# Performance work log

Hardware: AMD Instinct MI355X
Metric: run time of the kernel (lower is better)

The kernel has to match this reference:

```python
import jax, jax.numpy as jnp
import numpy as np
import math

HEAD_DIM = 128
N_HEADS = 32
N_KV_HEADS = 8
ROPE_THETA = 10000.0


def _rotate_half(x):
    x1, x2 = jnp.split(x, 2, axis=-1)
    return jnp.concatenate([-x2, x1], axis=-1)


def _rope_cos_sin(position_ids, head_dim, theta):
    # position_ids: [B, S] int
    inv_freq = 1.0 / (theta ** (jnp.arange(0, head_dim, 2, dtype=jnp.float32) / head_dim))
    freqs = position_ids.astype(jnp.float32)[..., None] * inv_freq[None, None, :]  # [B,S,D/2]
    emb = jnp.concatenate([freqs, freqs], axis=-1)  # [B,S,D]
    return jnp.cos(emb), jnp.sin(emb)


def setup_inputs() -> dict:
    key = jax.random.key(0)
    k1, k2, k3, k4, k5 = jax.random.split(key, 5)
    B, S, H = 1, 2048, 4096
    hidden_states = jax.random.normal(k1, (B, S, H), dtype=jnp.float32)
    Wq = jax.random.normal(k2, (N_HEADS * HEAD_DIM, H), dtype=jnp.float32) * (1.0 / math.sqrt(H))
    Wk = jax.random.normal(k3, (N_KV_HEADS * HEAD_DIM, H), dtype=jnp.float32) * (1.0 / math.sqrt(H))
    Wv = jax.random.normal(k4, (N_KV_HEADS * HEAD_DIM, H), dtype=jnp.float32) * (1.0 / math.sqrt(H))
    Wo = jax.random.normal(k5, (H, N_HEADS * HEAD_DIM), dtype=jnp.float32) * (1.0 / math.sqrt(H))
    position_ids = jnp.arange(S, dtype=jnp.int32)[None, :]
    return {"hidden_states": hidden_states, "Wq": Wq, "Wk": Wk, "Wv": Wv, "Wo": Wo,
            "position_ids": position_ids}


def reference(hidden_states, Wq, Wk, Wv, Wo, position_ids):
    B, S, H = hidden_states.shape
    d = HEAD_DIM
    groups = N_HEADS // N_KV_HEADS

    # projections (torch Linear: x @ W^T)
    q = (hidden_states @ Wq.T).reshape(B, S, N_HEADS, d).transpose(0, 2, 1, 3)      # [B,Hq,S,d]
    k = (hidden_states @ Wk.T).reshape(B, S, N_KV_HEADS, d).transpose(0, 2, 1, 3)   # [B,Hk,S,d]
    v = (hidden_states @ Wv.T).reshape(B, S, N_KV_HEADS, d).transpose(0, 2, 1, 3)

    cos, sin = _rope_cos_sin(position_ids, d, ROPE_THETA)  # [B,S,d]
    cos = cos[:, None, :, :]
    sin = sin[:, None, :, :]
    q = q * cos + _rotate_half(q) * sin
    k = k * cos + _rotate_half(k) * sin

    # GQA: repeat kv heads
    k = jnp.repeat(k, groups, axis=1)  # [B,Hq,S,d]
    v = jnp.repeat(v, groups, axis=1)

    scores = jnp.einsum('bhqd,bhkd->bhqk', q, k) / math.sqrt(d)
    causal = jnp.tril(jnp.ones((S, S), dtype=bool))
    scores = jnp.where(causal[None, None], scores, jnp.finfo(jnp.float32).min)
    attn = jax.nn.softmax(scores.astype(jnp.float32), axis=-1).astype(q.dtype)

    out = jnp.einsum('bhqk,bhkd->bhqd', attn, v)        # [B,Hq,S,d]
    out = out.transpose(0, 2, 1, 3).reshape(B, S, N_HEADS * d)
    return out @ Wo.T
```

## Files before the change

kernel.cpp:

```cpp
#include <hip/hip_runtime.h>
#include <hip/hip_bf16.h>
#include <cstdint>
#include <cstddef>

#define S_LEN 2048
#define HID   4096
#define HD    128
#define NH    32
#define NKV   8
#define KVW   (NKV * HD)
#define QKVN  (HID + 2 * KVW)

typedef __bf16 bf16x8_t __attribute__((ext_vector_type(8)));
typedef float  f32x4_t  __attribute__((ext_vector_type(4)));
typedef unsigned short u16x8_t __attribute__((ext_vector_type(8)));

__device__ __forceinline__ unsigned short f2b(float f) {
  unsigned u = __float_as_uint(f);
  u += 0x7FFFu + ((u >> 16) & 1u);
  return (unsigned short)(u >> 16);
}
__device__ __forceinline__ float b2f(unsigned short v) {
  return __uint_as_float(((unsigned)v) << 16);
}
__device__ __forceinline__ float fexp2(float x) {
  float r;
  asm("v_exp_f32 %0, %1" : "=v"(r) : "v"(x));
  return r;
}
__device__ __forceinline__ void gld_lds16(const void* g, void* l) {
  __builtin_amdgcn_global_load_lds(
      (const __attribute__((address_space(1))) void*)g,
      (__attribute__((address_space(3))) void*)l, 16, 0, 0);
}

__global__ void cvt4_kernel(const float* __restrict__ s0, const float* __restrict__ s1,
                            const float* __restrict__ s2, const float* __restrict__ s3,
                            unsigned short* __restrict__ dst) {
  const int B0 = 2097152;
  const int B1 = B0 + 4194304;
  const int B2 = B1 + 1048576;
  const int B3 = B2 + 1048576;
  int i = blockIdx.x * blockDim.x + threadIdx.x;
  int stride = gridDim.x * blockDim.x;
  for (; i < B3; i += stride) {
    const float* s; int off;
    if (i < B0)      { s = s0; off = i; }
    else if (i < B1) { s = s1; off = i - B0; }
    else if (i < B2) { s = s2; off = i - B1; }
    else             { s = s3; off = i - B2; }
    float4 v = reinterpret_cast<const float4*>(s)[off];
    ushort4 o;
    o.x = f2b(v.x); o.y = f2b(v.y); o.z = f2b(v.z); o.w = f2b(v.w);
    reinterpret_cast<ushort4*>(dst)[i] = o;
  }
}

#define QSCALE 0.12751744846f
__global__ void rope_kernel(unsigned short* __restrict__ Q,
                            unsigned short* __restrict__ Kb,
                            const int* __restrict__ pos_ids) {
  const int total = S_LEN * (NH + NKV) * 64;
  int idx = blockIdx.x * blockDim.x + threadIdx.x;
  int stride = gridDim.x * blockDim.x;
  for (; idx < total; idx += stride) {
    int s   = idx / ((NH + NKV) * 64);
    int rem = idx % ((NH + NKV) * 64);
    int hp  = rem >> 6;
    int i   = rem & 63;
    unsigned short* ptr; int W, h;
    if (hp < NH) { ptr = Q;  W = HID; h = hp; }
    else         { ptr = Kb; W = KVW; h = hp - NH; }
    float pos = (float)pos_ids[s];
    float ang = pos * __expf(-(float)i * 0.14391156516f);
    float sn, cs;
    sincosf(ang, &sn, &cs);
    size_t base = (size_t)s * W + (size_t)h * HD + i;
    float lo = b2f(ptr[base]);
    float hi = b2f(ptr[base + 64]);
    float o0 = lo * cs - hi * sn;
    float o1 = hi * cs + lo * sn;
    if (hp < NH) { o0 *= QSCALE; o1 *= QSCALE; }
    ptr[base]      = f2b(o0);
    ptr[base + 64] = f2b(o1);
  }
}

template <int BN, int MODE>
__global__ __launch_bounds__(512, 4) void gemm4p_kernel(
    const unsigned short* __restrict__ A, const unsigned short* __restrict__ B,
    void* __restrict__ C0, void* __restrict__ C1, void* __restrict__ C2,
    int N, int K) {
  constexpr int NFR = BN / 64;
  constexpr int ABYTES = 128 * 128;
  constexpr int TILE_LDS = ABYTES + BN * 128;
  __shared__ char ldsB[2 * TILE_LDS];

  const int tid  = threadIdx.x;
  const int lane = tid & 63;
  const int wid  = tid >> 6;
  const int wm = wid >> 2, wn = wid & 3;
  const int lr = lane & 15, g = lane >> 4;
  const int bm = blockIdx.y * 128;
  const int bn = blockIdx.x * BN;
  const int nk = K >> 6;
  const int ni = nk >> 1;
  const int xr = (lr & 7) << 4;

  auto stage_u = [&](int t, int u) {
    if (t >= nk) return;
    const int riu = tid >> 3;
    const int cbs = ((tid & 7) << 4) ^ ((riu & 7) << 4);
    const char* src;
    if (u < 2)
      src = (const char*)A + ((size_t)(bm + u * 64 + riu) * K + t * 64) * 2 + cbs;
    else
      src = (const char*)B + ((size_t)(bn + (u - 2) * 64 + riu) * K + t * 64) * 2 + cbs;
    gld_lds16(src, ldsB + (t & 1) * TILE_LDS + u * 8192 + tid * 16);
  };

  auto rdA = [&](const char* bb, int m, int k) {
    const int row = wm * 64 + m * 16 + lr;
    return *(const bf16x8_t*)(bb + row * 128 + ((k * 64 + g * 16) ^ xr));
  };
  auto rdB = [&](const char* bb, int n, int k) {
    const int row = wn * (BN / 4) + n * 16 + lr;
    return *(const bf16x8_t*)(bb + ABYTES + row * 128 + ((k * 64 + g * 16) ^ xr));
  };

  for (int t = 0; t < 2; ++t)
    for (int u = 0; u < 2 + NFR; ++u) stage_u(t, u);
  asm volatile("s_waitcnt vmcnt(0)" ::: "memory");
  __builtin_amdgcn_sched_barrier(0);
  __builtin_amdgcn_s_barrier();

  f32x4_t acc[4][NFR];
#pragma unroll
  for (int m = 0; m < 4; ++m)
#pragma unroll
    for (int n = 0; n < NFR; ++n) acc[m][n] = f32x4_t{0.f, 0.f, 0.f, 0.f};

  bf16x8_t bfr[NFR][2], af[2][2];

#define MFMA_BLOCK(MB)                                                        \
  __builtin_amdgcn_s_setprio(1);                                              \
  _Pragma("unroll") for (int m = 0; m < 2; ++m)                               \
    _Pragma("unroll") for (int n = 0; n < NFR; ++n)                           \
      _Pragma("unroll") for (int k = 0; k < 2; ++k)                           \
        acc[(MB) + m][n] = __builtin_amdgcn_mfma_f32_16x16x32_bf16(           \
            af[m][k], bfr[n][k], acc[(MB) + m][n], 0, 0, 0);                  \
  __builtin_amdgcn_s_setprio(0);

#define GATE()                                                                \
  __builtin_amdgcn_s_barrier();                                               \
  asm volatile("s_waitcnt lgkmcnt(0)" ::: "memory");                          \
  __builtin_amdgcn_sched_barrier(0);

#define RD_A2(bb, m0)                                                         \
  _Pragma("unroll") for (int m = 0; m < 2; ++m)                               \
    _Pragma("unroll") for (int k = 0; k < 2; ++k)                             \
      af[m][k] = rdA(bb, (m0) + m, k);

#define RD_B(bb)                                                              \
  _Pragma("unroll") for (int n = 0; n < NFR; ++n)                             \
    _Pragma("unroll") for (int k = 0; k < 2; ++k)                             \
      bfr[n][k] = rdB(bb, n, k);

  for (int i = 0; i < ni; ++i) {
    const char* bE = ldsB;
    const char* bO = ldsB + TILE_LDS;
    const int tO = 2 * i + 1, tE2 = 2 * i + 2, tO2 = 2 * i + 3;
    const bool last = (i == ni - 1);

    RD_B(bE);
    RD_A2(bE, 0);
    if (i > 0) { stage_u(tO, 0); stage_u(tO, 1); }
    GATE(); MFMA_BLOCK(0);
    __builtin_amdgcn_s_barrier();

    RD_A2(bE, 2);
#pragma unroll
    for (int u = 0; u < NFR; ++u) stage_u(tE2, 2 + u);
    GATE(); MFMA_BLOCK(2);
    if (last) { asm volatile("s_waitcnt vmcnt(0)" ::: "memory"); }
    else      { asm volatile("s_waitcnt vmcnt(%0)" :: "n"(NFR) : "memory"); }
    __builtin_amdgcn_sched_barrier(0);
    __builtin_amdgcn_s_barrier();

    RD_B(bO);
    RD_A2(bO, 0);
    stage_u(tE2, 0); stage_u(tE2, 1);
    GATE(); MFMA_BLOCK(0);
    __builtin_amdgcn_s_barrier();

    RD_A2(bO, 2);
#pragma unroll
    for (int u = 0; u < NFR; ++u) stage_u(tO2, 2 + u);
    GATE(); MFMA_BLOCK(2);
    if (!last) { asm volatile("s_waitcnt vmcnt(%0)" :: "n"(NFR) : "memory"); }
    __builtin_amdgcn_sched_barrier(0);
    __builtin_amdgcn_s_barrier();
  }
#undef MFMA_BLOCK
#undef GATE
#undef RD_A2
#undef RD_B

#pragma unroll
  for (int mf = 0; mf < 4; ++mf) {
    const int row0 = bm + wm * 64 + mf * 16 + g * 4;
#pragma unroll
    for (int nf = 0; nf < NFR; ++nf) {
      const int col = bn + wn * (BN / 4) + nf * 16 + lr;
      if constexpr (MODE == 1) {
#pragma unroll
        for (int r = 0; r < 4; ++r)
          ((float*)C0)[(size_t)(row0 + r) * N + col] = acc[mf][nf][r];
      } else {
        if (col < HID) {
#pragma unroll
          for (int r = 0; r < 4; ++r)
            ((unsigned short*)C0)[(size_t)(row0 + r) * HID + col] = f2b(acc[mf][nf][r]);
        } else if (col < HID + KVW) {
#pragma unroll
          for (int r = 0; r < 4; ++r)
            ((unsigned short*)C1)[(size_t)(row0 + r) * KVW + (col - HID)] = f2b(acc[mf][nf][r]);
        } else {
          const int c2 = col - HID - KVW;
          ushort4 w;
          w.x = f2b(acc[mf][nf][0]); w.y = f2b(acc[mf][nf][1]);
          w.z = f2b(acc[mf][nf][2]); w.w = f2b(acc[mf][nf][3]);
          *(ushort4*)(void*)&((unsigned short*)C2)[(size_t)c2 * S_LEN + row0] = w;
        }
      }
    }
  }
}

template <int BN, int MODE>
__global__ __launch_bounds__(256, 2) void gemm4w_kernel(
    const unsigned short* __restrict__ A, const unsigned short* __restrict__ B,
    void* __restrict__ C0, void* __restrict__ C1, void* __restrict__ C2,
    int N, int K) {
  constexpr int NFRW = BN / 32;
  constexpr int ABYTES = 128 * 128;
  constexpr int TILE_LDS = ABYTES + BN * 128;
  __shared__ char ldsB[2 * TILE_LDS];

  const int tid  = threadIdx.x;
  const int lane = tid & 63;
  const int wid  = tid >> 6;
  const int wm = wid >> 1, wn = wid & 1;
  const int lr = lane & 15, g = lane >> 4;
  const int bm = blockIdx.y * 128;
  const int bn = blockIdx.x * BN;
  const int nk = K >> 6;
  const int ni = nk >> 1;
  const int xr = (lr & 7) << 4;

  auto stage_u = [&](int t, int u) {
    if (t >= nk) return;
    const int riu = tid >> 3;
    const int cbs = ((tid & 7) << 4) ^ ((riu & 7) << 4);
    const char* src;
    if (u < 4)
      src = (const char*)A + ((size_t)(bm + u * 32 + riu) * K + t * 64) * 2 + cbs;
    else
      src = (const char*)B + ((size_t)(bn + (u - 4) * 32 + riu) * K + t * 64) * 2 + cbs;
    gld_lds16(src, ldsB + (t & 1) * TILE_LDS + u * 4096 + tid * 16);
  };

  auto rdA = [&](const char* bb, int m, int k) {
    const int row = wm * 64 + m * 16 + lr;
    return *(const bf16x8_t*)(bb + row * 128 + ((k * 64 + g * 16) ^ xr));
  };
  auto rdB = [&](const char* bb, int n, int k) {
    const int row = wn * (BN / 2) + n * 16 + lr;
    return *(const bf16x8_t*)(bb + ABYTES + row * 128 + ((k * 64 + g * 16) ^ xr));
  };

  for (int t = 0; t < 2; ++t)
    for (int u = 0; u < 4 + NFRW; ++u) stage_u(t, u);
  asm volatile("s_waitcnt vmcnt(0)" ::: "memory");
  __builtin_amdgcn_sched_barrier(0);
  __builtin_amdgcn_s_barrier();

  f32x4_t acc[4][NFRW];
#pragma unroll
  for (int m = 0; m < 4; ++m)
#pragma unroll
    for (int n = 0; n < NFRW; ++n) acc[m][n] = f32x4_t{0.f, 0.f, 0.f, 0.f};

  bf16x8_t bfr[NFRW][2], af[2][2];

#define MFMA_BLOCK(MB)                                                        \
  __builtin_amdgcn_s_setprio(1);                                              \
  _Pragma("unroll") for (int m = 0; m < 2; ++m)                               \
    _Pragma("unroll") for (int n = 0; n < NFRW; ++n)                          \
      _Pragma("unroll") for (int k = 0; k < 2; ++k)                           \
        acc[(MB) + m][n] = __builtin_amdgcn_mfma_f32_16x16x32_bf16(           \
            af[m][k], bfr[n][k], acc[(MB) + m][n], 0, 0, 0);                  \
  __builtin_amdgcn_s_setprio(0);

#define GATE()                                                                \
  __builtin_amdgcn_s_barrier();                                               \
  asm volatile("s_waitcnt lgkmcnt(0)" ::: "memory");                          \
  __builtin_amdgcn_sched_barrier(0);

#define RD_A2(bb, m0)                                                         \
  _Pragma("unroll") for (int m = 0; m < 2; ++m)                               \
    _Pragma("unroll") for (int k = 0; k < 2; ++k)                             \
      af[m][k] = rdA(bb, (m0) + m, k);

#define RD_B(bb)                                                              \
  _Pragma("unroll") for (int n = 0; n < NFRW; ++n)                            \
    _Pragma("unroll") for (int k = 0; k < 2; ++k)                             \
      bfr[n][k] = rdB(bb, n, k);

  for (int i = 0; i < ni; ++i) {
    const char* bE = ldsB;
    const char* bO = ldsB + TILE_LDS;
    const int tO = 2 * i + 1, tE2 = 2 * i + 2, tO2 = 2 * i + 3;
    const bool last = (i == ni - 1);

    RD_B(bE);
    RD_A2(bE, 0);
    if (i > 0) {
#pragma unroll
      for (int u = 0; u < 4; ++u) stage_u(tO, u);
    }
    GATE(); MFMA_BLOCK(0);
    __builtin_amdgcn_s_barrier();

    RD_A2(bE, 2);
#pragma unroll
    for (int u = 0; u < NFRW; ++u) stage_u(tE2, 4 + u);
    GATE(); MFMA_BLOCK(2);
    if (last) { asm volatile("s_waitcnt vmcnt(0)" ::: "memory"); }
    else      { asm volatile("s_waitcnt vmcnt(%0)" :: "n"(NFRW) : "memory"); }
    __builtin_amdgcn_sched_barrier(0);
    __builtin_amdgcn_s_barrier();

    RD_B(bO);
    RD_A2(bO, 0);
#pragma unroll
    for (int u = 0; u < 4; ++u) stage_u(tE2, u);
    GATE(); MFMA_BLOCK(0);
    __builtin_amdgcn_s_barrier();

    RD_A2(bO, 2);
#pragma unroll
    for (int u = 0; u < NFRW; ++u) stage_u(tO2, 4 + u);
    GATE(); MFMA_BLOCK(2);
    if (!last) { asm volatile("s_waitcnt vmcnt(%0)" :: "n"(NFRW) : "memory"); }
    __builtin_amdgcn_sched_barrier(0);
    __builtin_amdgcn_s_barrier();
  }
#undef MFMA_BLOCK
#undef GATE
#undef RD_A2
#undef RD_B

#pragma unroll
  for (int mf = 0; mf < 4; ++mf) {
    const int row0 = bm + wm * 64 + mf * 16 + g * 4;
#pragma unroll
    for (int nf = 0; nf < NFRW; ++nf) {
      const int col = bn + wn * (BN / 2) + nf * 16 + lr;
      if constexpr (MODE == 1) {
#pragma unroll
        for (int r = 0; r < 4; ++r)
          ((float*)C0)[(size_t)(row0 + r) * N + col] = acc[mf][nf][r];
      } else {
        if (col < HID) {
#pragma unroll
          for (int r = 0; r < 4; ++r)
            ((unsigned short*)C0)[(size_t)(row0 + r) * HID + col] = f2b(acc[mf][nf][r]);
        } else if (col < HID + KVW) {
#pragma unroll
          for (int r = 0; r < 4; ++r)
            ((unsigned short*)C1)[(size_t)(row0 + r) * KVW + (col - HID)] = f2b(acc[mf][nf][r]);
        } else {
          const int c2 = col - HID - KVW;
          ushort4 w;
          w.x = f2b(acc[mf][nf][0]); w.y = f2b(acc[mf][nf][1]);
          w.z = f2b(acc[mf][nf][2]); w.w = f2b(acc[mf][nf][3]);
          *(ushort4*)(void*)&((unsigned short*)C2)[(size_t)c2 * S_LEN + row0] = w;
        }
      }
    }
  }
}

__global__ __launch_bounds__(256) void attn_kernel(
    const unsigned short* __restrict__ Q, const unsigned short* __restrict__ K,
    const unsigned short* __restrict__ VtG, unsigned short* __restrict__ O,
    const float* __restrict__ WoF, unsigned short* __restrict__ WoB) {
  __shared__ char KlB[2][16384];
  __shared__ char VtB2[2][16384];
  __shared__ unsigned short Pl[4][16][72];

  const int tid  = threadIdx.x;
  const int lane = tid & 63;
  const int wave = tid >> 6;
  const int h    = blockIdx.y;
  const int kvh  = h >> 2;
  const int pair = blockIdx.x;
  const int lr   = lane & 15;
  const int g    = lane >> 4;
  const int lk8  = g * 8;
  const int blkl = h * 16 + pair;
  const int CVT_LIM = (HID * HID) / 4;
  int itg = 0;
  int pendidx = 0x7FFFFFFF;
  float4 pend;

  auto stageK = [&](int kv0, int buf) {
#pragma unroll
    for (int j = 0; j < 4; ++j) {
      const int row  = j * 16 + (tid >> 4);
      const int colb = ((tid & 15) << 4) ^ ((row & 15) << 4);
      const char* src =
          (const char*)(K + (size_t)(kv0 + row) * KVW + (size_t)kvh * HD) + colb;
      gld_lds16(src, &KlB[buf][row * 256 + ((tid & 15) << 4)]);
    }
  };
  auto stageV = [&](int kv0, int buf) {
#pragma unroll
    for (int j = 0; j < 4; ++j) {
      const int row  = j * 32 + (tid >> 3);
      const int colb = ((tid & 7) << 4) ^ ((row & 7) << 4);
      const char* src =
          (const char*)(VtG + ((size_t)kvh * HD + row) * S_LEN + kv0) + colb;
      gld_lds16(src, &VtB2[buf][row * 128 + ((tid & 7) << 4)]);
    }
  };
  auto rdK = [&](int buf, int n, int c) {
    const int row = n * 16 + lr;
    return *(const bf16x8_t*)&KlB[buf][row * 256 +
                                       ((c * 64 + g * 16) ^ ((lr & 15) << 4))];
  };
  auto rdV = [&](int buf, int c, int half) {
    const int row = c * 16 + lr;
    return *(const bf16x8_t*)&VtB2[buf][row * 128 +
                                        ((half * 64 + g * 16) ^ ((lr & 7) << 4))];
  };

  for (int pass = 0; pass < 2; ++pass) {
    const int qb = pass == 0 ? (31 - pair) : pair;
    const int q0 = qb * 64;
    const int qrow = q0 + wave * 16;
    const int nkv = qb + 1;

    bf16x8_t qf[4];
    {
      const unsigned short* qp = Q + (size_t)(qrow + lr) * HID + (size_t)h * HD;
#pragma unroll
      for (int c = 0; c < 4; ++c)
        qf[c] = *(const bf16x8_t*)(const void*)(qp + c * 32 + lk8);
    }
    f32x4_t oacc[8];
#pragma unroll
    for (int c = 0; c < 8; ++c) oacc[c] = f32x4_t{0.f, 0.f, 0.f, 0.f};
    float m_run = -3e38f, l_run = 0.f;

    stageK(0, 0); stageV(0, 0);
    asm volatile("s_waitcnt vmcnt(0)" ::: "memory");
    __builtin_amdgcn_sched_barrier(0);
    __builtin_amdgcn_s_barrier();

    for (int it = 0; it < nkv; ++it) {
      const int kv0 = it * 64;
      const int buf = it & 1;

      if (pendidx < CVT_LIM) {
        ushort4 o;
        o.x = f2b(pend.x); o.y = f2b(pend.y);
        o.z = f2b(pend.z); o.w = f2b(pend.w);
        reinterpret_cast<ushort4*>(WoB)[pendidx] = o;
      }
      pendidx = (blkl * 33 + itg) * 256 + tid;
      ++itg;
      if (pendidx < CVT_LIM)
        pend = reinterpret_cast<const float4*>(WoF)[pendidx];

      if (it + 1 < nkv) { stageK(kv0 + 64, buf ^ 1); stageV(kv0 + 64, buf ^ 1); }

      f32x4_t sacc[4];
#pragma unroll
      for (int n = 0; n < 4; ++n) sacc[n] = f32x4_t{0.f, 0.f, 0.f, 0.f};
#pragma unroll
      for (int c = 0; c < 4; ++c) {
        bf16x8_t qc = qf[c];
#pragma unroll
        for (int n = 0; n < 4; ++n)
          sacc[n] = __builtin_amdgcn_mfma_f32_16x16x32_bf16(rdK(buf, n, c), qc,
                                                            sacc[n], 0, 0, 0);
      }

      const int qg = qrow + lr;
      const bool diag = (it == nkv - 1);
      float p[16];
      float mloc = -3e38f;
#pragma unroll
      for (int n = 0; n < 4; ++n)
#pragma unroll
        for (int r = 0; r < 4; ++r) {
          float x = sacc[n][r];
          if (diag) {
            int kg = kv0 + n * 16 + g * 4 + r;
            if (kg > qg) x = -3e38f;
          }
          p[n * 4 + r] = x;
          mloc = fmaxf(mloc, x);
        }
      mloc = fmaxf(mloc, __shfl_xor(mloc, 16));
      mloc = fmaxf(mloc, __shfl_xor(mloc, 32));

      if (__any(mloc > m_run + 8.f)) {
        float m_new = fmaxf(m_run, mloc);
        float alpha = fexp2(m_run - m_new);
        float a4[4];
#pragma unroll
        for (int r = 0; r < 4; ++r) a4[r] = __shfl(alpha, g * 4 + r);
#pragma unroll
        for (int c = 0; c < 8; ++c)
#pragma unroll
          for (int r = 0; r < 4; ++r) oacc[c][r] *= a4[r];
        l_run *= alpha;
        m_run = m_new;
      }

      float ssum = 0.f;
#pragma unroll
      for (int i = 0; i < 16; ++i) {
        float e = fexp2(p[i] - m_run);
        p[i] = e;
        ssum += e;
      }
      ssum += __shfl_xor(ssum, 16);
      ssum += __shfl_xor(ssum, 32);
      l_run += ssum;

#pragma unroll
      for (int n = 0; n < 4; ++n) {
        ushort4 w;
        w.x = f2b(p[n * 4 + 0]); w.y = f2b(p[n * 4 + 1]);
        w.z = f2b(p[n * 4 + 2]); w.w = f2b(p[n * 4 + 3]);
        *(ushort4*)(void*)&Pl[wave][lr][n * 16 + g * 4] = w;
      }

#pragma unroll
      for (int half = 0; half < 2; ++half) {
        bf16x8_t pf = *(const bf16x8_t*)(const void*)&Pl[wave][lr][half * 32 + lk8];
#pragma unroll
        for (int c = 0; c < 8; ++c)
          oacc[c] = __builtin_amdgcn_mfma_f32_16x16x32_bf16(pf, rdV(buf, c, half),
                                                            oacc[c], 0, 0, 0);
      }

      if (it + 1 < nkv) { asm volatile("s_waitcnt vmcnt(0)" ::: "memory"); }
      __builtin_amdgcn_sched_barrier(0);
      __builtin_amdgcn_s_barrier();
    }

    float linv[4];
#pragma unroll
    for (int r = 0; r < 4; ++r) linv[r] = 1.f / __shfl(l_run, g * 4 + r);
#pragma unroll
    for (int r = 0; r < 4; ++r) {
      int row = qrow + g * 4 + r;
#pragma unroll
      for (int c = 0; c < 8; ++c)
        O[(size_t)row * HID + (size_t)h * HD + c * 16 + lr] = f2b(oacc[c][r] * linv[r]);
    }
  }

  if (pendidx < CVT_LIM) {
    ushort4 o;
    o.x = f2b(pend.x); o.y = f2b(pend.y);
    o.z = f2b(pend.z); o.w = f2b(pend.w);
    reinterpret_cast<ushort4*>(WoB)[pendidx] = o;
  }
}

extern "C" void kernel_launch(void* const* d_in, const int* in_sizes, int n_in,
                              void* d_out, int out_size, void* d_ws, size_t ws_size,
                              hipStream_t stream) {
  (void)in_sizes; (void)n_in; (void)out_size; (void)ws_size;
  const float* X  = (const float*)d_in[0];
  const float* Wq = (const float*)d_in[1];
  const float* Wk = (const float*)d_in[2];
  const float* Wv = (const float*)d_in[3];
  const float* Wo = (const float*)d_in[4];
  const int*  pos = (const int*)d_in[5];
  float* out = (float*)d_out;

  unsigned short* Xb  = (unsigned short*)d_ws;
  unsigned short* Wqb = Xb  + (size_t)S_LEN * HID;
  unsigned short* Wkb = Wqb + (size_t)HID * HID;
  unsigned short* Wvb = Wkb + (size_t)KVW * HID;
  unsigned short* Wob = Wvb + (size_t)KVW * HID;
  unsigned short* Qb  = Wob + (size_t)HID * HID;
  unsigned short* Kb  = Qb  + (size_t)S_LEN * HID;
  unsigned short* VtB = Kb  + (size_t)S_LEN * KVW;
  unsigned short* AOb = VtB + (size_t)S_LEN * KVW;

  cvt4_kernel<<<2048, 256, 0, stream>>>(X, Wq, Wk, Wv, Xb);

  gemm4p_kernel<192, 2><<<dim3(QKVN / 192, S_LEN / 128), 512, 0, stream>>>(
      Xb, Wqb, Qb, Kb, VtB, QKVN, HID);

  rope_kernel<<<2048, 256, 0, stream>>>(Qb, Kb, pos);

  attn_kernel<<<dim3(16, NH), 256, 0, stream>>>(Qb, Kb, VtB, AOb, Wo, Wob);

  gemm4w_kernel<128, 1><<<dim3(HID / 128, S_LEN / 128), 256, 0, stream>>>(
      AOb, Wob, out, nullptr, nullptr, HID, HID);
}
```

Baseline: 276.1 us.

## Split attention waves 2x2 over query and key halves with LDS merge

Waves in the attention block were each assigned 16 query rows across all 64 keys. They are now laid out as a 2x2 grid, each covering 32 query rows against 32 keys, so every K/V fragment read from LDS feeds two MFMAs. Each wave keeps separate online-softmax state for its key half, and at the end the two halves are merged through LDS using max/sum rescaling. This cuts LDS fragment reads per MFMA but doubles per-wave accumulator registers and adds a cross-wave reduction with extra barriers per pass.

```diff
diff --git a/kernel.cpp b/kernel.cpp
--- a/kernel.cpp
+++ b/kernel.cpp
@@ -398,11 +398,13 @@
     const float* __restrict__ WoF, unsigned short* __restrict__ WoB) {
   __shared__ char KlB[2][16384];
   __shared__ char VtB2[2][16384];
-  __shared__ unsigned short Pl[4][16][72];
+  __shared__ unsigned short Pl[4][2][16][40];
 
   const int tid  = threadIdx.x;
   const int lane = tid & 63;
   const int wave = tid >> 6;
+  const int qh   = wave >> 1;
+  const int kh   = wave & 1;
   const int h    = blockIdx.y;
   const int kvh  = h >> 2;
   const int pair = blockIdx.x;
@@ -435,34 +437,38 @@
       gld_lds16(src, &VtB2[buf][row * 128 + ((tid & 7) << 4)]);
     }
   };
-  auto rdK = [&](int buf, int n, int c) {
-    const int row = n * 16 + lr;
+  auto rdK = [&](int buf, int kf, int c) {
+    const int row = kh * 32 + kf * 16 + lr;
     return *(const bf16x8_t*)&KlB[buf][row * 256 +
-                                       ((c * 64 + g * 16) ^ ((lr & 15) << 4))];
-  };
-  auto rdV = [&](int buf, int c, int half) {
+                                       ((c * 64 + g * 16) ^ (lr << 4))];
+  };
+  auto rdV = [&](int buf, int c) {
     const int row = c * 16 + lr;
     return *(const bf16x8_t*)&VtB2[buf][row * 128 +
-                                        ((half * 64 + g * 16) ^ ((lr & 7) << 4))];
+                                        ((kh * 64 + g * 16) ^ ((lr & 7) << 4))];
   };
 
   for (int pass = 0; pass < 2; ++pass) {
     const int qb = pass == 0 ? (31 - pair) : pair;
     const int q0 = qb * 64;
-    const int qrow = q0 + wave * 16;
     const int nkv = qb + 1;
 
-    bf16x8_t qf[4];
-    {
-      const unsigned short* qp = Q + (size_t)(qrow + lr) * HID + (size_t)h * HD;
+    bf16x8_t qf[2][4];
+#pragma unroll
+    for (int qq = 0; qq < 2; ++qq) {
+      const unsigned short* qp =
+          Q + (size_t)(q0 + qh * 32 + qq * 16 + lr) * HID + (size_t)h * HD;
 #pragma unroll
       for (int c = 0; c < 4; ++c)
-        qf[c] = *(const bf16x8_t*)(const void*)(qp + c * 32 + lk8);
-    }
-    f32x4_t oacc[8];
-#pragma unroll
-    for (int c = 0; c < 8; ++c) oacc[c] = f32x4_t{0.f, 0.f, 0.f, 0.f};
-    float m_run = -3e38f, l_run = 0.f;
+        qf[qq][c] = *(const bf16x8_t*)(const void*)(qp + c * 32 + lk8);
+    }
+    f32x4_t oacc[2][8];
+#pragma unroll
+    for (int qq = 0; qq < 2; ++qq)
+#pragma unroll
+      for (int c = 0; c < 8; ++c) oacc[qq][c] = f32x4_t{0.f, 0.f, 0.f, 0.f};
+    float m_run[2] = {-1e30f, -1e30f};
+    float l_run[2] = {0.f, 0.f};
 
     stageK(0, 0); stageV(0, 0);
     asm volatile("s_waitcnt vmcnt(0)" ::: "memory");
@@ -486,77 +492,91 @@
 
       if (it + 1 < nkv) { stageK(kv0 + 64, buf ^ 1); stageV(kv0 + 64, buf ^ 1); }
 
-      f32x4_t sacc[4];
-#pragma unroll
-      for (int n = 0; n < 4; ++n) sacc[n] = f32x4_t{0.f, 0.f, 0.f, 0.f};
+      f32x4_t sacc[2][2];
+#pragma unroll
+      for (int qq = 0; qq < 2; ++qq)
+#pragma unroll
+        for (int kf = 0; kf < 2; ++kf) sacc[qq][kf] = f32x4_t{0.f, 0.f, 0.f, 0.f};
 #pragma unroll
       for (int c = 0; c < 4; ++c) {
-        bf16x8_t qc = qf[c];
-#pragma unroll
-        for (int n = 0; n < 4; ++n)
-          sacc[n] = __builtin_amdgcn_mfma_f32_16x16x32_bf16(rdK(buf, n, c), qc,
-                                                            sacc[n], 0, 0, 0);
-      }
-
-      const int qg = qrow + lr;
+        bf16x8_t k0 = rdK(buf, 0, c), k1 = rdK(buf, 1, c);
+#pragma unroll
+        for (int qq = 0; qq < 2; ++qq) {
+          sacc[qq][0] = __builtin_amdgcn_mfma_f32_16x16x32_bf16(k0, qf[qq][c], sacc[qq][0], 0, 0, 0);
+          sacc[qq][1] = __builtin_amdgcn_mfma_f32_16x16x32_bf16(k1, qf[qq][c], sacc[qq][1], 0, 0, 0);
+        }
+      }
+
       const bool diag = (it == nkv - 1);
-      float p[16];
-      float mloc = -3e38f;
-#pragma unroll
-      for (int n = 0; n < 4; ++n)
-#pragma unroll
-        for (int r = 0; r < 4; ++r) {
-          float x = sacc[n][r];
-          if (diag) {
-            int kg = kv0 + n * 16 + g * 4 + r;
-            if (kg > qg) x = -3e38f;
+      float p[2][8];
+      float mloc[2] = {-3e38f, -3e38f};
+#pragma unroll
+      for (int qq = 0; qq < 2; ++qq) {
+        const int qg = q0 + qh * 32 + qq * 16 + lr;
+#pragma unroll
+        for (int kf = 0; kf < 2; ++kf)
+#pragma unroll
+          for (int r = 0; r < 4; ++r) {
+            float x = sacc[qq][kf][r];
+            if (diag) {
+              int kg = kv0 + kh * 32 + kf * 16 + g * 4 + r;
+              if (kg > qg) x = -3e38f;
+            }
+            p[qq][kf * 4 + r] = x;
+            mloc[qq] = fmaxf(mloc[qq], x);
           }
-          p[n * 4 + r] = x;
-          mloc = fmaxf(mloc, x);
-        }
-      mloc = fmaxf(mloc, __shfl_xor(mloc, 16));
-      mloc = fmaxf(mloc, __shfl_xor(mloc, 32));
-
-      if (__any(mloc > m_run + 8.f)) {
-        float m_new = fmaxf(m_run, mloc);
-        float alpha = fexp2(m_run - m_new);
-        float a4[4];
-#pragma unroll
-        for (int r = 0; r < 4; ++r) a4[r] = __shfl(alpha, g * 4 + r);
+        mloc[qq] = fmaxf(mloc[qq], __shfl_xor(mloc[qq], 16));
+        mloc[qq] = fmaxf(mloc[qq], __shfl_xor(mloc[qq], 32));
+      }
+
+      if (__any((mloc[0] > m_run[0] + 8.f) || (mloc[1] > m_run[1] + 8.f))) {
+#pragma unroll
+        for (int qq = 0; qq < 2; ++qq) {
+          float m_new = fmaxf(m_run[qq], mloc[qq]);
+          float alpha = fexp2(m_run[qq] - m_new);
+          float a4[4];
+#pragma unroll
+          for (int r = 0; r < 4; ++r) a4[r] = __shfl(alpha, g * 4 + r);
+#pragma unroll
+          for (int c = 0; c < 8; ++c)
+#pragma unroll
+            for (int r = 0; r < 4; ++r) oacc[qq][c][r] *= a4[r];
+          l_run[qq] *= alpha;
+          m_run[qq] = m_new;
+        }
+      }
+
+#pragma unroll
+      for (int qq = 0; qq < 2; ++qq) {
+        float ssum = 0.f;
+#pragma unroll
+        for (int i = 0; i < 8; ++i) {
+          float e = fexp2(p[qq][i] - m_run[qq]);
+          p[qq][i] = e;
+          ssum += e;
+        }
+        ssum += __shfl_xor(ssum, 16);
+        ssum += __shfl_xor(ssum, 32);
+        l_run[qq] += ssum;
+      }
+
+#pragma unroll
+      for (int qq = 0; qq < 2; ++qq)
+#pragma unroll
+        for (int kf = 0; kf < 2; ++kf) {
+          ushort4 w;
+          w.x = f2b(p[qq][kf * 4 + 0]); w.y = f2b(p[qq][kf * 4 + 1]);
+          w.z = f2b(p[qq][kf * 4 + 2]); w.w = f2b(p[qq][kf * 4 + 3]);
+          *(ushort4*)(void*)&Pl[wave][qq][lr][kf * 16 + g * 4] = w;
+        }
+
+#pragma unroll
+      for (int qq = 0; qq < 2; ++qq) {
+        bf16x8_t pf = *(const bf16x8_t*)(const void*)&Pl[wave][qq][lr][g * 8];
 #pragma unroll
         for (int c = 0; c < 8; ++c)
-#pragma unroll
-          for (int r = 0; r < 4; ++r) oacc[c][r] *= a4[r];
-        l_run *= alpha;
-        m_run = m_new;
-      }
-
-      float ssum = 0.f;
-#pragma unroll
-      for (int i = 0; i < 16; ++i) {
-        float e = fexp2(p[i] - m_run);
-        p[i] = e;
-        ssum += e;
-      }
-      ssum += __shfl_xor(ssum, 16);
-      ssum += __shfl_xor(ssum, 32);
-      l_run += ssum;
-
-#pragma unroll
-      for (int n = 0; n < 4; ++n) {
-        ushort4 w;
-        w.x = f2b(p[n * 4 + 0]); w.y = f2b(p[n * 4 + 1]);
-        w.z = f2b(p[n * 4 + 2]); w.w = f2b(p[n * 4 + 3]);
-        *(ushort4*)(void*)&Pl[wave][lr][n * 16 + g * 4] = w;
-      }
-
-#pragma unroll
-      for (int half = 0; half < 2; ++half) {
-        bf16x8_t pf = *(const bf16x8_t*)(const void*)&Pl[wave][lr][half * 32 + lk8];
-#pragma unroll
-        for (int c = 0; c < 8; ++c)
-          oacc[c] = __builtin_amdgcn_mfma_f32_16x16x32_bf16(pf, rdV(buf, c, half),
-                                                            oacc[c], 0, 0, 0);
+          oacc[qq][c] = __builtin_amdgcn_mfma_f32_16x16x32_bf16(pf, rdV(buf, c),
+                                                               oacc[qq][c], 0, 0, 0);
       }
 
       if (it + 1 < nkv) { asm volatile("s_waitcnt vmcnt(0)" ::: "memory"); }
@@ -564,16 +584,48 @@
       __builtin_amdgcn_s_barrier();
     }
 
-    float linv[4];
-#pragma unroll
-    for (int r = 0; r < 4; ++r) linv[r] = 1.f / __shfl(l_run, g * 4 + r);
-#pragma unroll
-    for (int r = 0; r < 4; ++r) {
-      int row = qrow + g * 4 + r;
-#pragma unroll
-      for (int c = 0; c < 8; ++c)
-        O[(size_t)row * HID + (size_t)h * HD + c * 16 + lr] = f2b(oacc[c][r] * linv[r]);
-    }
+    if (kh == 1) {
+      float* mlp = (float*)&VtB2[0][0] + (qh * 64 + lane) * 4;
+      mlp[0] = m_run[0]; mlp[1] = l_run[0];
+      mlp[2] = m_run[1]; mlp[3] = l_run[1];
+      float* op = (float*)&KlB[0][0] + qh * 4096 + lane * 64;
+#pragma unroll
+      for (int qq = 0; qq < 2; ++qq)
+#pragma unroll
+        for (int c = 0; c < 8; ++c)
+#pragma unroll
+          for (int r = 0; r < 4; ++r)
+            op[qq * 32 + c * 4 + r] = oacc[qq][c][r];
+    }
+    __builtin_amdgcn_s_barrier();
+    if (kh == 0) {
+      const float* mlp = (const float*)&VtB2[0][0] + (qh * 64 + lane) * 4;
+      const float* op  = (const float*)&KlB[0][0] + qh * 4096 + lane * 64;
+#pragma unroll
+      for (int qq = 0; qq < 2; ++qq) {
+        float m1 = mlp[qq * 2 + 0], l1 = mlp[qq * 2 + 1];
+        float ms = fmaxf(m_run[qq], m1);
+        float w0 = fexp2(m_run[qq] - ms), w1 = fexp2(m1 - ms);
+        float linv = 1.f / (l_run[qq] * w0 + l1 * w1);
+        float s0 = w0 * linv, s1 = w1 * linv;
+        float s0r[4], s1r[4];
+#pragma unroll
+        for (int r = 0; r < 4; ++r) {
+          s0r[r] = __shfl(s0, g * 4 + r);
+          s1r[r] = __shfl(s1, g * 4 + r);
+        }
+#pragma unroll
+        for (int r = 0; r < 4; ++r) {
+          const int row = q0 + qh * 32 + qq * 16 + g * 4 + r;
+#pragma unroll
+          for (int c = 0; c < 8; ++c) {
+            float o = oacc[qq][c][r] * s0r[r] + op[qq * 32 + c * 4 + r] * s1r[r];
+            O[(size_t)row * HID + (size_t)h * HD + c * 16 + lr] = f2b(o);
+          }
+        }
+      }
+    }
+    __builtin_amdgcn_s_barrier();
   }
 
   if (pendidx < CVT_LIM) {
```

New measurement: 337.0 us. 22.0% more time.
